# Optimization experiments

Measured on AMD Instinct MI355X. Metric: run time of the kernel, lower is better.

The kernel has to match this reference:

```python
import jax, jax.numpy as jnp
import numpy as np

D_MODEL = 1024; D_INNER = 2048; HEADDIM = 64; NHEADS = 32; DSTATE = 128
NGROUPS = 1; DCONV = 4; CHUNK = 256; EPS = 1e-5
D_IN_PROJ = 2 * D_INNER + 2 * NGROUPS * DSTATE + NHEADS
CONV_DIM = D_INNER + 2 * NGROUPS * DSTATE
B_SZ = 2; L_SEQ = 4096


def segsum(x):
    # x: (..., T) -> (..., T, T) lower-triangular segment sums (off-diag = -inf)
    T = x.shape[-1]
    cs = jnp.cumsum(x, axis=-1)
    ss = cs[..., :, None] - cs[..., None, :]
    return jnp.where(jnp.tril(jnp.ones((T, T), bool)), ss, -jnp.inf)


def ssd(x, dt, A, Bm, Cm):
    # Chunked SSD selective scan (Mamba2). x:(b,l,h,p) dt:(b,l,h) A:(h,) Bm,Cm:(b,l,g,n)
    b, l, h, p = x.shape
    c = l // CHUNK
    x = x.reshape(b, c, CHUNK, h, p)
    dt = dt.reshape(b, c, CHUNK, h)
    rep = h // NGROUPS
    Bh = jnp.repeat(Bm.reshape(b, c, CHUNK, NGROUPS, DSTATE), rep, axis=3)
    Ch = jnp.repeat(Cm.reshape(b, c, CHUNK, NGROUPS, DSTATE), rep, axis=3)
    xdt = x * dt[..., None]                       # discretized input dt*x
    Adt = (dt * A).transpose(0, 3, 1, 2)          # (b,h,c,T)
    A_cs = jnp.cumsum(Adt, axis=-1)
    Lmat = jnp.exp(segsum(Adt))                   # (b,h,c,T,T) intra-chunk decays
    Y_diag = jnp.einsum('bcthn,bcshn,bhcts,bcshp->bcthp', Ch, Bh, Lmat, xdt)
    decay_states = jnp.exp(A_cs[..., -1:] - A_cs)  # (b,h,c,T)
    states = jnp.einsum('bcthn,bhct,bcthp->bchpn', Bh, decay_states, xdt)
    A_pad = jnp.pad(A_cs[..., -1], ((0, 0), (0, 0), (1, 0)))  # (b,h,c+1)
    decay_chunk = jnp.exp(segsum(A_pad))          # (b,h,c+1,c+1) inter-chunk recurrence
    states = jnp.concatenate([jnp.zeros_like(states[:, :1]), states], axis=1)
    prev = jnp.einsum('bhzc,bchpn->bzhpn', decay_chunk, states)[:, :-1]
    Y_off = jnp.einsum('bcthn,bchpn,bhct->bcthp', Ch, prev, jnp.exp(A_cs))
    return (Y_diag + Y_off).reshape(b, l, h, p)


def mamba_dir(zxbcdt, conv_w, conv_b, dt_bias, A_log, Dp, norm_w):
    # One direction of mamba_split_conv1d_scan_combined (silu act, gated RMSNorm).
    b, l, _ = zxbcdt.shape
    z = zxbcdt[..., :D_INNER]
    xBC = zxbcdt[..., D_INNER:D_INNER + CONV_DIM]
    dt_raw = zxbcdt[..., D_INNER + CONV_DIM:]
    # causal depthwise conv1d (kernel=DCONV) + silu
    xp = jnp.pad(xBC, ((0, 0), (DCONV - 1, 0), (0, 0)))
    conv = conv_b
    for k in range(DCONV):
        conv = conv + conv_w[:, k] * xp[:, k:k + l, :]
    xBC = jax.nn.silu(conv)
    x = xBC[..., :D_INNER].reshape(b, l, NHEADS, HEADDIM)
    Bm = xBC[..., D_INNER:D_INNER + NGROUPS * DSTATE].reshape(b, l, NGROUPS, DSTATE)
    Cm = xBC[..., D_INNER + NGROUPS * DSTATE:].reshape(b, l, NGROUPS, DSTATE)
    dt = jax.nn.softplus(dt_raw + dt_bias)        # (b,l,h)
    A = -jnp.exp(A_log.astype(jnp.float32))       # (h,)
    y = ssd(x, dt, A, Bm, Cm) + x * Dp[None, None, :, None]  # D skip on raw x
    y = y.reshape(b, l, D_INNER)
    y = y * jax.nn.silu(z)                        # gate BEFORE norm (norm_before_gate=False)
    y = y * jax.lax.rsqrt(jnp.mean(y * y, axis=-1, keepdims=True) + EPS) * norm_w
    return y


def setup_inputs():
    rng = np.random.default_rng(0)
    f32 = lambda a: jnp.asarray(a, jnp.float32)
    # dt_bias init per BiMamba2.__init__
    dt = np.exp(rng.uniform(size=NHEADS) * (np.log(0.1) - np.log(0.001)) + np.log(0.001))
    dt = np.clip(dt, 1e-4, None)
    inv_dt = dt + np.log(-np.expm1(-dt))
    A_log = np.log(rng.uniform(1.0, 16.0, NHEADS))
    return dict(
        u=f32(rng.standard_normal((B_SZ, L_SEQ, D_MODEL))),
        in_proj_w=f32(rng.standard_normal((D_IN_PROJ, D_MODEL)) * 0.02),
        conv_w=f32(rng.standard_normal((CONV_DIM, DCONV)) * 0.2),
        conv_b=f32(np.zeros(CONV_DIM)),
        dt_bias=f32(inv_dt),
        A_log=f32(A_log),
        D=f32(np.ones(NHEADS)),
        norm_w=f32(np.ones(D_INNER)),
        bi_conv_w=f32(rng.standard_normal((CONV_DIM, DCONV)) * 0.2),
        bi_conv_b=f32(np.zeros(CONV_DIM)),
        bi_dt_bias=f32(inv_dt.copy()),
        bi_A_log=f32(A_log.copy()),
        bi_D=f32(np.ones(NHEADS)),
        bi_norm_w=f32(np.ones(D_INNER)),
        out_proj_w=f32(rng.standard_normal((D_MODEL, D_INNER)) * 0.02),
    )


def reference(u, in_proj_w, conv_w, conv_b, dt_bias, A_log, D, norm_w,
              bi_conv_w, bi_conv_b, bi_dt_bias, bi_A_log, bi_D, bi_norm_w, out_proj_w):
    zxbcdt = jnp.einsum('bld,ed->ble', u, in_proj_w)
    fwd = mamba_dir(zxbcdt, conv_w, conv_b, dt_bias, A_log, D, norm_w)
    bwd = mamba_dir(zxbcdt[:, ::-1], bi_conv_w, bi_conv_b, bi_dt_bias, bi_A_log, bi_D, bi_norm_w)
    out = (fwd + bwd[:, ::-1]) * 0.5
    return jnp.einsum('ble,de->bld', out, out_proj_w)
```

## Files before the change

kernel.cpp:

```cpp
#include <hip/hip_runtime.h>

#define LSEQ 4096
#define BSZ 2
#define DMODEL 1024
#define DINNER 2048
#define NHEADS 32
#define HEADDIM 64
#define DSTATE 128
#define CHUNK 256
#define NCHUNK 16
#define CONVDIM 2304
#define DINPROJ 4384
#define NPAD 4480
#define BL (BSZ*LSEQ)

typedef unsigned short u16;
typedef unsigned int u32;
typedef u16 u16x4 __attribute__((ext_vector_type(4)));
typedef u16 u16x8 __attribute__((ext_vector_type(8)));
typedef __bf16 bf16x8 __attribute__((ext_vector_type(8)));
typedef float f32x4 __attribute__((ext_vector_type(4)));

__device__ __forceinline__ u16 f2bf(float f){
  union { float f; u32 u; } v; v.f = f;
  u32 r = v.u + 0x7fffu + ((v.u >> 16) & 1u);
  return (u16)(r >> 16);
}
__device__ __forceinline__ float bf2f(u16 h){
  union { u32 u; float f; } v; v.u = ((u32)h) << 16;
  return v.f;
}
__device__ __forceinline__ u32 pack2(float a, float b){
  return (u32)f2bf(a) | ((u32)f2bf(b) << 16);
}
__device__ __forceinline__ f32x4 mfma16(bf16x8 a, bf16x8 b, f32x4 c){
  return __builtin_amdgcn_mfma_f32_16x16x32_bf16(a, b, c, 0, 0, 0);
}
__device__ __forceinline__ void gload16(const void* g, void* l){
  __builtin_amdgcn_global_load_lds((const __attribute__((address_space(1))) void*)g,
                                   (__attribute__((address_space(3))) void*)l, 16, 0, 0);
}

__global__ void sentinel_kernel(float* out){ out[threadIdx.x] = 123456.0f; }

__global__ void cvt_kernel(const float* __restrict__ in, u16* __restrict__ out,
                           long nin, long nout){
  long i = (long)blockIdx.x*blockDim.x + threadIdx.x;
  long stride = (long)gridDim.x*blockDim.x;
  for (; i < nout; i += stride) out[i] = (i < nin) ? f2bf(in[i]) : (u16)0;
}

template<int BF16OUT>
__global__ __launch_bounds__(256) void gemm_bt(const u16* __restrict__ A, const u16* __restrict__ B,
                                               void* __restrict__ Cv, int K, int ldc)
{
  __shared__ u16 As[4096];
  __shared__ u16 Bs[4096];
  const int tid = threadIdx.x, lane = tid & 63;
  const int wave = tid >> 6;
  const int wr = wave >> 1, wc = wave & 1;
  f32x4 acc[4][4];
  #pragma unroll
  for (int i=0;i<4;i++)
    #pragma unroll
    for (int j=0;j<4;j++) acc[i][j] = (f32x4){0.f,0.f,0.f,0.f};

  const u16* Ag = A + (size_t)blockIdx.x * 128 * K;
  const u16* Bg = B + (size_t)blockIdx.y * 128 * K;
  const u16* srcG = ((wave < 2) ? Ag : Bg) + (size_t)((wave & 1) * 64) * K;
  u16* dstL = ((wave < 2) ? As : Bs) + (wave & 1) * 64 * 32;
  const int lrow = lane >> 2;
  const int scol = ((lane & 3) ^ ((lane >> 3) & 3));
  const int r = lane & 15, g = lane >> 4;
  const int sg = (g ^ ((r >> 1) & 3)) * 8;

  for (int kt = 0; kt < K; kt += 32) {
    __syncthreads();
    #pragma unroll
    for (int i=0;i<4;i++){
      const u16* gp = srcG + (size_t)(i*16 + lrow)*K + kt + scol*8;
      gload16(gp, dstL + i*512);
    }
    __syncthreads();
    bf16x8 af[4], bfv[4];
    #pragma unroll
    for (int mt=0;mt<4;mt++) af[mt] = *(const bf16x8*)&As[(wr*64+mt*16+r)*32 + sg];
    #pragma unroll
    for (int nt=0;nt<4;nt++) bfv[nt] = *(const bf16x8*)&Bs[(wc*64+nt*16+r)*32 + sg];
    #pragma unroll
    for (int mt=0;mt<4;mt++)
      #pragma unroll
      for (int nt=0;nt<4;nt++)
        acc[mt][nt] = mfma16(af[mt], bfv[nt], acc[mt][nt]);
  }
  const size_t cbase = (size_t)(blockIdx.x*128 + wr*64 + g*4) * ldc
                     + blockIdx.y*128 + wc*64 + r;
  if (BF16OUT) {
    u16* Cg = (u16*)Cv + cbase;
    #pragma unroll
    for (int mt=0;mt<4;mt++)
      #pragma unroll
      for (int nt=0;nt<4;nt++)
        #pragma unroll
        for (int j=0;j<4;j++)
          Cg[(size_t)(mt*16+j)*ldc + nt*16] = f2bf(acc[mt][nt][j]);
  } else {
    float* Cg = (float*)Cv + cbase;
    #pragma unroll
    for (int mt=0;mt<4;mt++)
      #pragma unroll
      for (int nt=0;nt<4;nt++)
        #pragma unroll
        for (int j=0;j<4;j++)
          Cg[(size_t)(mt*16+j)*ldc + nt*16] = acc[mt][nt][j];
  }
}

__global__ __launch_bounds__(320) void conv_kernel(
    const u16* __restrict__ zxh, const float* __restrict__ cw, const float* __restrict__ cb,
    const float* __restrict__ dtb,
    u16* __restrict__ xout, u16* __restrict__ Bout, u16* __restrict__ Cout,
    float* __restrict__ dtt, int rev)
{
  const int l = blockIdx.x, b = blockIdx.y, tid = threadIdx.x;
  if (tid < 288){
    const int ch0 = tid*8;
    f32x4 cw4[8];
    #pragma unroll
    for (int j=0;j<8;j++) cw4[j] = *(const f32x4*)&cw[(ch0+j)*4];
    float acc[8];
    {
      f32x4 b0 = *(const f32x4*)&cb[ch0];
      f32x4 b1 = *(const f32x4*)&cb[ch0+4];
      #pragma unroll
      for (int j=0;j<4;j++){ acc[j] = b0[j]; acc[4+j] = b1[j]; }
    }
    #pragma unroll
    for (int k=0;k<4;k++){
      int ls = l - 3 + k;
      if (ls >= 0){
        int lsrc = rev ? (LSEQ-1-ls) : ls;
        u16x8 v = *(const u16x8*)(zxh + ((size_t)b*LSEQ + lsrc)*NPAD + DINNER + ch0);
        #pragma unroll
        for (int j=0;j<8;j++) acc[j] += cw4[j][k] * bf2f(v[j]);
      }
    }
    u16x8 o;
    #pragma unroll
    for (int j=0;j<8;j++){
      float sv = acc[j] / (1.f + __expf(-acc[j]));
      o[j] = f2bf(sv);
    }
    if (ch0 < DINNER)
      *(u16x8*)(xout + ((size_t)b*LSEQ + l)*DINNER + ch0) = o;
    else if (ch0 < DINNER+DSTATE)
      *(u16x8*)(Bout + ((size_t)b*LSEQ + l)*DSTATE + (ch0 - DINNER)) = o;
    else
      *(u16x8*)(Cout + ((size_t)b*LSEQ + l)*DSTATE + (ch0 - DINNER - DSTATE)) = o;
  } else {
    const int hh = tid - 288;
    const int lsrc = rev ? (LSEQ-1-l) : l;
    float raw = bf2f(zxh[((size_t)b*LSEQ + lsrc)*NPAD + DINNER + CONVDIM + hh]) + dtb[hh];
    float dv = (raw > 20.f) ? raw : log1pf(__expf(raw));
    dtt[((size_t)b*NHEADS + hh)*LSEQ + l] = dv;
  }
}

__global__ __launch_bounds__(256) void acs_kernel(const float* __restrict__ dtt,
    const float* __restrict__ A_log, float* __restrict__ acs)
{
  const int c = blockIdx.x, hh = blockIdx.y, b = blockIdx.z;
  const int t = threadIdx.x;
  __shared__ float s[CHUNK];
  const float Ah = -__expf(A_log[hh]);
  const size_t base = ((size_t)b*NHEADS + hh)*LSEQ + (size_t)c*CHUNK;
  s[t] = dtt[base + t] * Ah;
  __syncthreads();
  for (int off=1; off<CHUNK; off<<=1){
    float add = (t >= off) ? s[t-off] : 0.f;
    __syncthreads();
    s[t] += add;
    __syncthreads();
  }
  acs[base + t] = s[t];
}

__global__ __launch_bounds__(256) void states_kernel(
    const u16* __restrict__ xb, const u16* __restrict__ Bb,
    const float* __restrict__ dtt, const float* __restrict__ acs,
    u16* __restrict__ states)
{
  const int h = blockIdx.x, c = blockIdx.y, b = blockIdx.z;
  const int tid = threadIdx.x, lane = tid & 63, w = tid >> 6;
  __shared__ float acs_s[CHUNK], dt_s[CHUNK];
  __shared__ u32 xdtTW[64*20];
  __shared__ u32 BsdW[128*20];

  const size_t bhBase = ((size_t)b*NHEADS + h)*LSEQ + (size_t)c*CHUNK;
  acs_s[tid] = acs[bhBase + tid];
  dt_s[tid]  = dtt[bhBase + tid];
  __syncthreads();
  const float acsLast = acs_s[CHUNK-1];

  f32x4 sacc[4][2];
  #pragma unroll
  for (int i=0;i<4;i++){ sacc[i][0] = (f32x4){0,0,0,0}; sacc[i][1] = (f32x4){0,0,0,0}; }

  const int s2 = tid >> 4, q = tid & 15;
  const int g = lane >> 4, r = lane & 15;
  const size_t rowBase = (size_t)b*LSEQ + (size_t)c*CHUNK;
  for (int st8 = 0; st8 < 8; ++st8) {
    const int s0 = st8*32;
    const int sA = s0 + 2*s2, sB = sA + 1;
    u16x4 xA = *(const u16x4*)(xb + (rowBase+sA)*DINNER + h*HEADDIM + 4*q);
    u16x4 xB4 = *(const u16x4*)(xb + (rowBase+sB)*DINNER + h*HEADDIM + 4*q);
    u16x8 bA = *(const u16x8*)(Bb + (rowBase+sA)*DSTATE + 8*q);
    u16x8 bB = *(const u16x8*)(Bb + (rowBase+sB)*DSTATE + 8*q);
    const float dA = dt_s[sA], dB = dt_s[sB];
    const float eA = __expf(acsLast - acs_s[sA]), eB = __expf(acsLast - acs_s[sB]);
    __syncthreads();
    #pragma unroll
    for (int j=0;j<4;j++){
      int p = 4*q + j;
      xdtTW[p*20 + (s2 ^ (((p>>3)&3)<<2))] = pack2(bf2f(xA[j])*dA, bf2f(xB4[j])*dB);
    }
    #pragma unroll
    for (int j=0;j<8;j++){
      int n = 8*q + j;
      BsdW[n*20 + (s2 ^ (((n>>3)&3)<<2))] = pack2(bf2f(bA[j])*eA, bf2f(bB[j])*eB);
    }
    __syncthreads();
    bf16x8 xf[4];
    #pragma unroll
    for (int pt=0;pt<4;pt++){
      int p = pt*16 + r;
      xf[pt] = *(const bf16x8*)&xdtTW[p*20 + 4*(g ^ ((p>>3)&3))];
    }
    #pragma unroll
    for (int nt=0;nt<2;nt++){
      int n = w*32 + nt*16 + r;
      bf16x8 bdf = *(const bf16x8*)&BsdW[n*20 + 4*(g ^ ((n>>3)&3))];
      #pragma unroll
      for (int pt=0;pt<4;pt++) sacc[pt][nt] = mfma16(xf[pt], bdf, sacc[pt][nt]);
    }
  }
  u16* sp = states + (((size_t)b*NCHUNK + c)*NHEADS + h)*(size_t)(HEADDIM*DSTATE);
  #pragma unroll
  for (int pt=0;pt<4;pt++)
    #pragma unroll
    for (int nt=0;nt<2;nt++)
      #pragma unroll
      for (int j=0;j<4;j++)
        sp[(size_t)(pt*16+g*4+j)*DSTATE + w*32+nt*16+r] = f2bf(sacc[pt][nt][j]);
}

__global__ __launch_bounds__(256) void recur_kernel(const u16* __restrict__ states,
    const float* __restrict__ acs, u16* __restrict__ prev)
{
  const int b = blockIdx.x >> 5, h = blockIdx.x & 31;
  const int tid = threadIdx.x;
  float S[32];
  #pragma unroll
  for (int k=0;k<32;k++) S[k] = 0.f;
  for (int c=0;c<NCHUNK;c++){
    const size_t off = (((size_t)b*NCHUNK + c)*NHEADS + h)*(size_t)(HEADDIM*DSTATE);
    const float dc = __expf(acs[((size_t)b*NHEADS+h)*LSEQ + (size_t)c*CHUNK + CHUNK-1]);
    #pragma unroll
    for (int k=0;k<32;k++){
      const size_t i = off + tid + k*256;
      prev[i] = f2bf(S[k]);
      S[k] = S[k]*dc + bf2f(states[i]);
    }
  }
}

__global__ __launch_bounds__(256) void ydiagoff_kernel(
    const u16* __restrict__ xb, const u16* __restrict__ Bb, const u16* __restrict__ Cb,
    const float* __restrict__ dtt, const float* __restrict__ acs,
    const u16* __restrict__ prev, const float* __restrict__ Dp,
    u16* __restrict__ ydir)
{
  const int h = blockIdx.x, c = blockIdx.y, b = blockIdx.z;
  const int tid = threadIdx.x, lane = tid & 63, w = tid >> 6;
  __shared__ float acs_s[CHUNK], dt_s[CHUNK];
  __shared__ u16 Bs[32][136];
  __shared__ u32 xdtTW[64*20];
  __shared__ u16 Ms[4][64][40];

  const size_t bhBase = ((size_t)b*NHEADS + h)*LSEQ + (size_t)c*CHUNK;
  acs_s[tid] = acs[bhBase + tid];
  dt_s[tid]  = dtt[bhBase + tid];
  __syncthreads();

  const int g = lane >> 4, r = lane & 15;
  const size_t rowBase = (size_t)b*LSEQ + (size_t)c*CHUNK;

  bf16x8 caf[4][4];
  const u16* Crow = Cb + rowBase*DSTATE;
  #pragma unroll
  for (int mt=0;mt<4;mt++)
    #pragma unroll
    for (int ks=0;ks<4;ks++)
      caf[mt][ks] = *(const bf16x8*)(Crow + (size_t)(mt*64+w*16+r)*DSTATE + ks*32 + g*8);

  f32x4 yacc[4][4];
  #pragma unroll
  for (int i=0;i<4;i++)
    #pragma unroll
    for (int j=0;j<4;j++) yacc[i][j] = (f32x4){0,0,0,0};

  const int sl = tid >> 3, part = tid & 7;
  const int s2 = tid >> 4, q = tid & 15;
  for (int st8 = 0; st8 < 8; ++st8) {
    const int s0 = st8*32;
    u16x8 v0 = *(const u16x8*)(Bb + (rowBase + s0 + sl)*DSTATE + part*16);
    u16x8 v1 = *(const u16x8*)(Bb + (rowBase + s0 + sl)*DSTATE + part*16 + 8);
    const int sA = s0 + 2*s2, sB = sA + 1;
    u16x4 xA = *(const u16x4*)(xb + (rowBase+sA)*DINNER + h*HEADDIM + 4*q);
    u16x4 xB4 = *(const u16x4*)(xb + (rowBase+sB)*DINNER + h*HEADDIM + 4*q);
    const float dA = dt_s[sA], dB = dt_s[sB];
    __syncthreads();
    *(u16x8*)&Bs[sl][part*16]   = v0;
    *(u16x8*)&Bs[sl][part*16+8] = v1;
    #pragma unroll
    for (int j=0;j<4;j++){
      int p = 4*q + j;
      xdtTW[p*20 + (s2 ^ (((p>>3)&3)<<2))] = pack2(bf2f(xA[j])*dA, bf2f(xB4[j])*dB);
    }
    __syncthreads();
    bf16x8 xf[4];
    #pragma unroll
    for (int pt=0;pt<4;pt++){
      int p = pt*16 + r;
      xf[pt] = *(const bf16x8*)&xdtTW[p*20 + 4*(g ^ ((p>>3)&3))];
    }
    #pragma unroll
    for (int mt=0;mt<4;mt++){
      if (4*mt + w >= 2*st8) {
        f32x4 g20 = (f32x4){0,0,0,0}, g21 = (f32x4){0,0,0,0};
        #pragma unroll
        for (int ks=0;ks<4;ks++){
          bf16x8 bfv0 = *(const bf16x8*)&Bs[r][ks*32+g*8];
          bf16x8 bfv1 = *(const bf16x8*)&Bs[16+r][ks*32+g*8];
          g20 = mfma16(caf[mt][ks], bfv0, g20);
          g21 = mfma16(caf[mt][ks], bfv1, g21);
        }
        #pragma unroll
        for (int j=0;j<4;j++){
          int tl = mt*64 + w*16 + g*4 + j;
          int sg0 = s0 + r;
          int sg1 = s0 + 16 + r;
          float m0 = (sg0 <= tl) ? g20[j]*__expf(acs_s[tl]-acs_s[sg0]) : 0.f;
          float m1 = (sg1 <= tl) ? g21[j]*__expf(acs_s[tl]-acs_s[sg1]) : 0.f;
          Ms[w][mt*16+g*4+j][r]    = f2bf(m0);
          Ms[w][mt*16+g*4+j][16+r] = f2bf(m1);
        }
        bf16x8 mf = *(const bf16x8*)&Ms[w][mt*16+r][g*8];
        #pragma unroll
        for (int pt=0;pt<4;pt++) yacc[mt][pt] = mfma16(mf, xf[pt], yacc[mt][pt]);
      }
    }
  }
  #pragma unroll
  for (int mt=0;mt<4;mt++){
    const float et = __expf(acs_s[mt*64 + w*16 + r]);
    #pragma unroll
    for (int ks=0;ks<4;ks++)
      #pragma unroll
      for (int e=0;e<8;e++)
        caf[mt][ks][e] = (__bf16)((float)caf[mt][ks][e] * et);
  }
  const u16* pv = prev + (((size_t)b*NCHUNK + c)*NHEADS + h)*(size_t)(HEADDIM*DSTATE);
  #pragma unroll
  for (int ks=0;ks<4;ks++){
    bf16x8 pf[4];
    #pragma unroll
    for (int pt=0;pt<4;pt++)
      pf[pt] = *(const bf16x8*)(pv + (size_t)(pt*16+r)*DSTATE + ks*32 + g*8);
    #pragma unroll
    for (int mt=0;mt<4;mt++)
      #pragma unroll
      for (int pt=0;pt<4;pt++) yacc[mt][pt] = mfma16(caf[mt][ks], pf[pt], yacc[mt][pt]);
  }
  const float Dh = Dp[h];
  const u16* xrow = xb + rowBase*DINNER + h*HEADDIM;
  u16* yrow = ydir + rowBase*DINNER + h*HEADDIM;
  #pragma unroll
  for (int mt=0;mt<4;mt++)
    #pragma unroll
    for (int pt=0;pt<4;pt++)
      #pragma unroll
      for (int j=0;j<4;j++){
        int tl = mt*64 + w*16 + g*4 + j;
        int p  = pt*16 + r;
        float xv = bf2f(xrow[(size_t)tl*DINNER + p]);
        yrow[(size_t)tl*DINNER + p] = f2bf(yacc[mt][pt][j] + xv*Dh);
      }
}

__global__ __launch_bounds__(256) void gate_norm_kernel(
    const u16* __restrict__ ydir, const u16* __restrict__ zxh,
    const float* __restrict__ nw, u16* __restrict__ ybufh, int rev)
{
  const int l = blockIdx.x, b = blockIdx.y, tid = threadIdx.x;
  const int lsrc = rev ? (LSEQ-1-l) : l;
  u16x8 zv = *(const u16x8*)(zxh + ((size_t)b*LSEQ + lsrc)*NPAD + tid*8);
  u16x8 yv = *(const u16x8*)(ydir + ((size_t)b*LSEQ + l)*DINNER + tid*8);
  float gg[8]; float ss = 0.f;
  #pragma unroll
  for (int j=0;j<8;j++){
    float z = bf2f(zv[j]);
    float y = bf2f(yv[j]);
    float v = y * (z / (1.f + __expf(-z)));
    gg[j] = v; ss += v*v;
  }
  #pragma unroll
  for (int off=32; off>0; off>>=1) ss += __shfl_xor(ss, off, 64);
  __shared__ float red[4];
  if ((tid&63)==0) red[tid>>6] = ss;
  __syncthreads();
  float tot = red[0]+red[1]+red[2]+red[3];
  float scale = rsqrtf(tot * (1.f/DINNER) + 1e-5f);
  const float* nwp = nw + tid*8;
  u16* hrow = ybufh + ((size_t)b*LSEQ + lsrc)*DINNER + tid*8;
  u16x8 o;
  if (!rev){
    #pragma unroll
    for (int j=0;j<8;j++) o[j] = f2bf(0.5f * gg[j]*scale*nwp[j]);
  } else {
    u16x8 pvv = *(const u16x8*)hrow;
    #pragma unroll
    for (int j=0;j<8;j++) o[j] = f2bf(bf2f(pvv[j]) + 0.5f*gg[j]*scale*nwp[j]);
  }
  *(u16x8*)hrow = o;
}

extern "C" void kernel_launch(void* const* d_in, const int* in_sizes, int n_in,
                              void* d_out, int out_size, void* d_ws, size_t ws_size,
                              hipStream_t stream) {
  const float* u        = (const float*)d_in[0];
  const float* w1       = (const float*)d_in[1];
  const float* conv_w   = (const float*)d_in[2];
  const float* conv_b   = (const float*)d_in[3];
  const float* dt_bias  = (const float*)d_in[4];
  const float* A_log    = (const float*)d_in[5];
  const float* Dp       = (const float*)d_in[6];
  const float* norm_w   = (const float*)d_in[7];
  const float* bconv_w  = (const float*)d_in[8];
  const float* bconv_b  = (const float*)d_in[9];
  const float* bdt_bias = (const float*)d_in[10];
  const float* bA_log   = (const float*)d_in[11];
  const float* bDp      = (const float*)d_in[12];
  const float* bnorm_w  = (const float*)d_in[13];
  const float* wo       = (const float*)d_in[14];
  float* out = (float*)d_out;

  const size_t SZ_ZX  = (size_t)BL*NPAD*2;
  const size_t SZ_UB  = (size_t)BL*DMODEL*2;
  const size_t SZ_W1  = (size_t)NPAD*DMODEL*2;
  const size_t SZ_WO  = (size_t)DMODEL*DINNER*2;
  const size_t SZ_XB  = (size_t)BL*DINNER*2;
  const size_t SZ_BB  = (size_t)BL*DSTATE*2;
  const size_t SZ_DT  = (size_t)BSZ*NHEADS*LSEQ*4;
  const size_t SZ_ST  = (size_t)BSZ*NCHUNK*NHEADS*HEADDIM*DSTATE*2;
  const size_t SZ_YD  = (size_t)BL*DINNER*2;
  const size_t SZ_YH  = (size_t)BL*DINNER*2;
  const size_t NEED = SZ_ZX + SZ_UB + SZ_W1 + SZ_WO + SZ_XB + 2*SZ_BB + 2*SZ_DT
                    + SZ_ST + SZ_YD + SZ_YH;
  if (ws_size < NEED) { sentinel_kernel<<<1,256,0,stream>>>(out); return; }

  char* p = (char*)d_ws;
  u16*   zxh    = (u16*)p;              p += SZ_ZX;
  u16*   ub     = (u16*)p;              p += SZ_UB;
  u16*   states = ub;
  u16*   w1b    = (u16*)p;              p += SZ_W1;
  u16*   wob    = (u16*)p;              p += SZ_WO;
  u16*   xb     = (u16*)p;              p += SZ_XB;
  u16*   Bb     = (u16*)p;              p += SZ_BB;
  u16*   Cb     = (u16*)p;              p += SZ_BB;
  float* dtt    = (float*)p;            p += SZ_DT;
  float* acs    = (float*)p;            p += SZ_DT;
  u16*   prev   = (u16*)p;              p += SZ_ST;
  u16*   ydir   = (u16*)p;              p += SZ_YD;
  u16*   ybufh  = (u16*)p;              p += SZ_YH;

  cvt_kernel<<<2048,256,0,stream>>>(u,  ub,  (long)BL*DMODEL,      (long)BL*DMODEL);
  cvt_kernel<<<2048,256,0,stream>>>(w1, w1b, (long)DINPROJ*DMODEL, (long)NPAD*DMODEL);
  cvt_kernel<<<2048,256,0,stream>>>(wo, wob, (long)DMODEL*DINNER,  (long)DMODEL*DINNER);

  gemm_bt<1><<<dim3(BL/128, NPAD/128),256,0,stream>>>(ub, w1b, zxh, DMODEL, NPAD);

  for (int dir = 0; dir < 2; ++dir) {
    const float* cwp = dir ? bconv_w  : conv_w;
    const float* cbp = dir ? bconv_b  : conv_b;
    const float* dbp = dir ? bdt_bias : dt_bias;
    const float* alp = dir ? bA_log   : A_log;
    const float* ddp = dir ? bDp      : Dp;
    const float* nwp = dir ? bnorm_w  : norm_w;
    conv_kernel<<<dim3(LSEQ,BSZ),320,0,stream>>>(zxh, cwp, cbp, dbp, xb, Bb, Cb, dtt, dir);
    acs_kernel<<<dim3(NCHUNK,NHEADS,BSZ),256,0,stream>>>(dtt, alp, acs);
    states_kernel<<<dim3(NHEADS,NCHUNK,BSZ),256,0,stream>>>(xb, Bb, dtt, acs, states);
    recur_kernel<<<BSZ*NHEADS,256,0,stream>>>(states, acs, prev);
    ydiagoff_kernel<<<dim3(NHEADS,NCHUNK,BSZ),256,0,stream>>>(xb, Bb, Cb, dtt, acs, prev, ddp, ydir);
    gate_norm_kernel<<<dim3(LSEQ,BSZ),256,0,stream>>>(ydir, zxh, nwp, ybufh, dir);
  }

  gemm_bt<0><<<dim3(BL/128, DMODEL/128),256,0,stream>>>(ybufh, wob, out, DINNER, DMODEL);
}
```

Before: 518.1 us.

## Deepen GEMM K-tile to 64, split recurrence across blocks, batch MFMAs in ydiag

The GEMM now stages 64-wide K tiles in shared memory with a new XOR swizzle, which halves the number of barrier pairs per K loop. The inter-chunk recurrence kernel splits each head's state into 8 segments over 8x more blocks, raising parallelism from 64 blocks. The ydiagoff kernel computes all C·B^T MFMA tiles for a step before the masking and decay pass, so B fragment loads are shared across mt and more MFMAs can be in flight. The costs are higher LDS use per GEMM block and more live registers in ydiagoff, which may lower occupancy.

```diff
diff --git a/kernel.cpp b/kernel.cpp
--- a/kernel.cpp
+++ b/kernel.cpp
@@ -54,8 +54,8 @@
 __global__ __launch_bounds__(256) void gemm_bt(const u16* __restrict__ A, const u16* __restrict__ B,
                                                void* __restrict__ Cv, int K, int ldc)
 {
-  __shared__ u16 As[4096];
-  __shared__ u16 Bs[4096];
+  __shared__ u16 As[128*64];
+  __shared__ u16 Bs[128*64];
   const int tid = threadIdx.x, lane = tid & 63;
   const int wave = tid >> 6;
   const int wr = wave >> 1, wc = wave & 1;
@@ -68,30 +68,34 @@
   const u16* Ag = A + (size_t)blockIdx.x * 128 * K;
   const u16* Bg = B + (size_t)blockIdx.y * 128 * K;
   const u16* srcG = ((wave < 2) ? Ag : Bg) + (size_t)((wave & 1) * 64) * K;
-  u16* dstL = ((wave < 2) ? As : Bs) + (wave & 1) * 64 * 32;
-  const int lrow = lane >> 2;
-  const int scol = ((lane & 3) ^ ((lane >> 3) & 3));
+  u16* dstL = ((wave < 2) ? As : Bs) + (wave & 1) * 64 * 64;
+  const int lrow8 = lane >> 3;
+  const int scol  = (lane & 7) ^ (lane >> 3);
   const int r = lane & 15, g = lane >> 4;
-  const int sg = (g ^ ((r >> 1) & 3)) * 8;
-
-  for (int kt = 0; kt < K; kt += 32) {
-    __syncthreads();
-    #pragma unroll
-    for (int i=0;i<4;i++){
-      const u16* gp = srcG + (size_t)(i*16 + lrow)*K + kt + scol*8;
+
+  for (int kt = 0; kt < K; kt += 64) {
+    __syncthreads();
+    #pragma unroll
+    for (int i=0;i<8;i++){
+      const u16* gp = srcG + (size_t)(i*8 + lrow8)*K + kt + scol*8;
       gload16(gp, dstL + i*512);
     }
     __syncthreads();
-    bf16x8 af[4], bfv[4];
-    #pragma unroll
-    for (int mt=0;mt<4;mt++) af[mt] = *(const bf16x8*)&As[(wr*64+mt*16+r)*32 + sg];
-    #pragma unroll
-    for (int nt=0;nt<4;nt++) bfv[nt] = *(const bf16x8*)&Bs[(wc*64+nt*16+r)*32 + sg];
-    #pragma unroll
-    for (int mt=0;mt<4;mt++)
+    #pragma unroll
+    for (int kk=0;kk<2;kk++){
+      bf16x8 af[4], bfv[4];
+      #pragma unroll
+      for (int mt=0;mt<4;mt++)
+        af[mt] = *(const bf16x8*)&As[(wr*64+mt*16+r)*64 + (((kk*4+g) ^ (r&7))*8)];
       #pragma unroll
       for (int nt=0;nt<4;nt++)
-        acc[mt][nt] = mfma16(af[mt], bfv[nt], acc[mt][nt]);
+        bfv[nt] = *(const bf16x8*)&Bs[(wc*64+nt*16+r)*64 + (((kk*4+g) ^ (r&7))*8)];
+      #pragma unroll
+      for (int mt=0;mt<4;mt++)
+        #pragma unroll
+        for (int nt=0;nt<4;nt++)
+          acc[mt][nt] = mfma16(af[mt], bfv[nt], acc[mt][nt]);
+    }
   }
   const size_t cbase = (size_t)(blockIdx.x*128 + wr*64 + g*4) * ldc
                      + blockIdx.y*128 + wc*64 + r;
@@ -257,16 +261,19 @@
 __global__ __launch_bounds__(256) void recur_kernel(const u16* __restrict__ states,
     const float* __restrict__ acs, u16* __restrict__ prev)
 {
-  const int b = blockIdx.x >> 5, h = blockIdx.x & 31;
+  const int bx = blockIdx.x;
+  const int seg = bx & 7, bh = bx >> 3;
+  const int b = bh >> 5, h = bh & 31;
   const int tid = threadIdx.x;
-  float S[32];
-  #pragma unroll
-  for (int k=0;k<32;k++) S[k] = 0.f;
+  float S[4];
+  #pragma unroll
+  for (int k=0;k<4;k++) S[k] = 0.f;
   for (int c=0;c<NCHUNK;c++){
-    const size_t off = (((size_t)b*NCHUNK + c)*NHEADS + h)*(size_t)(HEADDIM*DSTATE);
+    const size_t off = (((size_t)b*NCHUNK + c)*NHEADS + h)*(size_t)(HEADDIM*DSTATE)
+                     + seg*1024;
     const float dc = __expf(acs[((size_t)b*NHEADS+h)*LSEQ + (size_t)c*CHUNK + CHUNK-1]);
     #pragma unroll
-    for (int k=0;k<32;k++){
+    for (int k=0;k<4;k++){
       const size_t i = off + tid + k*256;
       prev[i] = f2bf(S[k]);
       S[k] = S[k]*dc + bf2f(states[i]);
@@ -328,6 +335,21 @@
       xdtTW[p*20 + (s2 ^ (((p>>3)&3)<<2))] = pack2(bf2f(xA[j])*dA, bf2f(xB4[j])*dB);
     }
     __syncthreads();
+    f32x4 g2[4][2];
+    #pragma unroll
+    for (int i=0;i<4;i++){ g2[i][0] = (f32x4){0,0,0,0}; g2[i][1] = (f32x4){0,0,0,0}; }
+    #pragma unroll
+    for (int ks=0;ks<4;ks++){
+      bf16x8 bfv0 = *(const bf16x8*)&Bs[r][ks*32+g*8];
+      bf16x8 bfv1 = *(const bf16x8*)&Bs[16+r][ks*32+g*8];
+      #pragma unroll
+      for (int mt=0;mt<4;mt++){
+        if (4*mt + w >= 2*st8) {
+          g2[mt][0] = mfma16(caf[mt][ks], bfv0, g2[mt][0]);
+          g2[mt][1] = mfma16(caf[mt][ks], bfv1, g2[mt][1]);
+        }
+      }
+    }
     bf16x8 xf[4];
     #pragma unroll
     for (int pt=0;pt<4;pt++){
@@ -337,21 +359,13 @@
     #pragma unroll
     for (int mt=0;mt<4;mt++){
       if (4*mt + w >= 2*st8) {
-        f32x4 g20 = (f32x4){0,0,0,0}, g21 = (f32x4){0,0,0,0};
-        #pragma unroll
-        for (int ks=0;ks<4;ks++){
-          bf16x8 bfv0 = *(const bf16x8*)&Bs[r][ks*32+g*8];
-          bf16x8 bfv1 = *(const bf16x8*)&Bs[16+r][ks*32+g*8];
-          g20 = mfma16(caf[mt][ks], bfv0, g20);
-          g21 = mfma16(caf[mt][ks], bfv1, g21);
-        }
         #pragma unroll
         for (int j=0;j<4;j++){
           int tl = mt*64 + w*16 + g*4 + j;
           int sg0 = s0 + r;
           int sg1 = s0 + 16 + r;
-          float m0 = (sg0 <= tl) ? g20[j]*__expf(acs_s[tl]-acs_s[sg0]) : 0.f;
-          float m1 = (sg1 <= tl) ? g21[j]*__expf(acs_s[tl]-acs_s[sg1]) : 0.f;
+          float m0 = (sg0 <= tl) ? g2[mt][0][j]*__expf(acs_s[tl]-acs_s[sg0]) : 0.f;
+          float m1 = (sg1 <= tl) ? g2[mt][1][j]*__expf(acs_s[tl]-acs_s[sg1]) : 0.f;
           Ms[w][mt*16+g*4+j][r]    = f2bf(m0);
           Ms[w][mt*16+g*4+j][16+r] = f2bf(m1);
         }
@@ -500,7 +514,7 @@
     conv_kernel<<<dim3(LSEQ,BSZ),320,0,stream>>>(zxh, cwp, cbp, dbp, xb, Bb, Cb, dtt, dir);
     acs_kernel<<<dim3(NCHUNK,NHEADS,BSZ),256,0,stream>>>(dtt, alp, acs);
     states_kernel<<<dim3(NHEADS,NCHUNK,BSZ),256,0,stream>>>(xb, Bb, dtt, acs, states);
-    recur_kernel<<<BSZ*NHEADS,256,0,stream>>>(states, acs, prev);
+    recur_kernel<<<BSZ*NHEADS*8,256,0,stream>>>(states, acs, prev);
     ydiagoff_kernel<<<dim3(NHEADS,NCHUNK,BSZ),256,0,stream>>>(xb, Bb, Cb, dtt, acs, prev, ddp, ydir);
     gate_norm_kernel<<<dim3(LSEQ,BSZ),256,0,stream>>>(ydir, zxh, nwp, ybufh, dir);
   }
```

Result: slower. 640.5 us (+23.6%).
